# Performance work log

Measured on AMD Instinct MI355X. Metric: run time of the kernel, lower is better.

Reference implementation:

```python
import jax, jax.numpy as jnp
import numpy as np

B, C, H, W, N = 4, 5, 256, 256, 2048
HW = H * W


def setup_inputs() -> dict:
    key = jax.random.key(0)
    ks = jax.random.split(key, 8)
    s = 1.0 / np.sqrt(C)
    x = jax.random.normal(ks[0], (B, C, H, W), jnp.float32)
    Wq = jax.random.normal(ks[1], (C, C), jnp.float32) * s
    Wk = jax.random.normal(ks[2], (C, C), jnp.float32) * s
    Wv = jax.random.normal(ks[3], (C, C), jnp.float32) * s
    bq = jnp.zeros((C,), jnp.float32)
    bk = jnp.zeros((C,), jnp.float32)
    bv = jnp.zeros((C,), jnp.float32)
    gamma = jnp.zeros((1,), jnp.float32)  # nn.Parameter(torch.zeros(1))
    idx_b = jax.random.randint(ks[4], (N,), 0, B, jnp.int32)
    idx_h = jax.random.randint(ks[5], (N,), 0, H, jnp.int32)
    idx_w = jax.random.randint(ks[6], (N,), 0, W, jnp.int32)
    return {"x": x, "Wq": Wq, "bq": bq, "Wk": Wk, "bk": bk, "Wv": Wv,
            "bv": bv, "gamma": gamma, "idx_b": idx_b, "idx_h": idx_h, "idx_w": idx_w}


def _conv1x1(x, Wt, b):
    # 1x1 conv == per-pixel channel mix
    return jnp.einsum('oc,bchw->bohw', Wt, x) + b[None, :, None, None]


def reference(x, Wq, bq, Wk, bk, Wv, bv, gamma, idx_b, idx_h, idx_w):
    q = _conv1x1(x, Wq, bq)
    k = _conv1x1(x, Wk, bk)
    v = _conv1x1(x, Wv, bv)
    q_pix = q[idx_b, :, idx_h, idx_w]              # [N, C] gathered query pixels
    Kf = k.reshape(B, C, HW)
    Vf = v.reshape(B, C, HW)
    # energy[n, l] = sum_c q_pix[n, c] * Kf[idx_b[n], c, l]
    # channel loop (C=5, fixed) avoids materializing [N, C, HW]
    energy = jnp.zeros((N, HW), x.dtype)
    for c in range(C):
        energy = energy + q_pix[:, c:c + 1] * Kf[idx_b, c]   # [N, HW]
    attn = jax.nn.softmax(energy, axis=-1)                   # [N, HW]
    out = jnp.stack([jnp.sum(Vf[idx_b, c] * attn, axis=-1) for c in range(C)],
                    axis=1)                                  # [N, C]
    upd = (gamma[0] + 0.1) * out + x[idx_b, :, idx_h, idx_w]
    # y starts as a detached copy of x; selected pixels are overwritten
    y = jax.lax.stop_gradient(x).at[idx_b, :, idx_h, idx_w].set(upd)
    return y
```

## Files before the change

kernel.cpp:

```cpp
#include <hip/hip_runtime.h>


constexpr int HWC = 256 * 256;
constexpr int Bc  = 4;
constexpr int Nq  = 2048;
constexpr int Wc  = 256;

constexpr int TPB   = 40;
constexpr int SPLIT = 16;

constexpr float LOG2E = 1.4426950408889634f;
constexpr float BIAS2 = -14.0f * LOG2E;

constexpr size_t K8_BYTES  = (size_t)Bc * HWC * 8 * 2;
constexpr size_t VT_BYTES  = (size_t)Bc * 5 * HWC * 2;
constexpr size_t QP_BYTES  = (size_t)Nq * 8 * 2;
constexpr size_t PART_BYTES = (size_t)SPLIT * Nq * 6 * 4;
constexpr size_t K8_OFF   = 0;
constexpr size_t VT_OFF   = K8_OFF + K8_BYTES;
constexpr size_t QP16_OFF = VT_OFF + VT_BYTES;
constexpr size_t PART_OFF = QP16_OFF + QP_BYTES;
constexpr size_t PERM_OFF = PART_OFF + PART_BYTES;
constexpr size_t CNT_OFF  = PERM_OFF + (size_t)Bc * Nq * 4;

typedef __attribute__((ext_vector_type(8))) _Float16 f16x8;
typedef __attribute__((ext_vector_type(4))) float f32x4;
union FU { uint4 u; f16x8 h; };

#if defined(__has_builtin)
#if __has_builtin(__builtin_amdgcn_exp2f)
#define EXP2F(x) __builtin_amdgcn_exp2f(x)
#endif
#endif
#ifndef EXP2F
#define EXP2F(x) exp2f(x)
#endif

__device__ inline unsigned pack2(float a, float b) {
  typedef __attribute__((ext_vector_type(2))) __fp16 fp16x2;
  union { fp16x2 h; unsigned u; } r;
  r.h = __builtin_amdgcn_cvt_pkrtz(a, b);
  return r.u;
}

__global__ __launch_bounds__(256) void k1_prep(
    const float* __restrict__ x,
    const float* __restrict__ Wq, const float* __restrict__ bq,
    const float* __restrict__ Wk, const float* __restrict__ bk,
    const float* __restrict__ Wv, const float* __restrict__ bv,
    const int* __restrict__ idx_b, const int* __restrict__ idx_h,
    const int* __restrict__ idx_w,
    float* __restrict__ y, char* __restrict__ wsb) {
  const int tid = threadIdx.x;
  _Float16* K8   = (_Float16*)(wsb + K8_OFF);
  _Float16* VT   = (_Float16*)(wsb + VT_OFF);
  _Float16* QP16 = (_Float16*)(wsb + QP16_OFF);
  if (blockIdx.x >= 1024) {
    if (blockIdx.x == 1032) {
      __shared__ int lcnt[Bc];
      if (tid < Bc) lcnt[tid] = 0;
      __syncthreads();
      int* perm = (int*)(wsb + PERM_OFF);
#pragma unroll
      for (int qi = 0; qi < 8; ++qi) {
        const int n = qi * 256 + tid;
        const int b = idx_b[n];
        const int pos = atomicAdd(&lcnt[b], 1);
        perm[b * Nq + pos] = n;
      }
      __syncthreads();
      if (tid < Bc) ((int*)(wsb + CNT_OFF))[tid] = lcnt[tid];
      return;
    }
    const int n = (blockIdx.x - 1024) * 256 + tid;
    const int b = idx_b[n];
    const int s = idx_h[n] * Wc + idx_w[n];
    float xv[5];
#pragma unroll
    for (int c = 0; c < 5; ++c) xv[c] = x[(size_t)(b * 5 + c) * HWC + s];
    float q[5];
#pragma unroll
    for (int o = 0; o < 5; ++o) {
      float t = bq[o];
#pragma unroll
      for (int c = 0; c < 5; ++c) t = fmaf(Wq[o * 5 + c], xv[c], t);
      q[o] = t * LOG2E;
    }
    uint4 row;
    row.x = pack2(q[0], q[1]);
    row.y = pack2(q[2], q[3]);
    row.z = pack2(q[4], 0.f);
    row.w = 0u;
    *(uint4*)(QP16 + (size_t)n * 8) = row;
    return;
  }
  const int gid = blockIdx.x * 256 + tid;
  const int b   = gid >> 16;
  const int s   = gid & (HWC - 1);
  float xv[5];
#pragma unroll
  for (int c = 0; c < 5; ++c) {
    const size_t off = (size_t)(b * 5 + c) * HWC + s;
    xv[c] = x[off];
    y[off] = xv[c];
  }
  float kk[5], vv[5];
#pragma unroll
  for (int o = 0; o < 5; ++o) {
    kk[o] = bk[o];
    vv[o] = bv[o];
#pragma unroll
    for (int c = 0; c < 5; ++c) {
      kk[o] = fmaf(Wk[o * 5 + c], xv[c], kk[o]);
      vv[o] = fmaf(Wv[o * 5 + c], xv[c], vv[o]);
    }
  }
  uint4 krow;
  krow.x = pack2(kk[0], kk[1]);
  krow.y = pack2(kk[2], kk[3]);
  krow.z = pack2(kk[4], 0.f);
  krow.w = 0u;
  *(uint4*)(K8 + (size_t)(b * HWC + s) * 8) = krow;
#pragma unroll
  for (int c = 0; c < 5; ++c)
    VT[(size_t)(b * 5 + c) * HWC + s] = (_Float16)vv[c];
}

__global__ __launch_bounds__(256) void k2_attn(char* __restrict__ wsb) {
  const int chunk = blockIdx.x;
  const int tile  = blockIdx.y;
  const int bb    = tile / TPB;
  const int tt    = tile % TPB;
  const int cb    = ((const int*)(wsb + CNT_OFF))[bb];
  const int j0    = tt * 16;
  if (j0 >= cb) return;
  const int* perm = (const int*)(wsb + PERM_OFF) + bb * Nq;

  const int tid  = threadIdx.x;
  const int wv   = tid >> 6;
  const int lane = tid & 63;
  const int quad = lane >> 4;
  const int l15  = lane & 15;

  __shared__ _Float16 Pbuf[4][16][64];
  __shared__ float    Ored[4][16][6];

  const _Float16* K8b  = (const _Float16*)(wsb + K8_OFF) + (size_t)bb * HWC * 8;
  const _Float16* Vtb  = (const _Float16*)(wsb + VT_OFF) + (size_t)bb * 5 * HWC;
  const _Float16* QP16 = (const _Float16*)(wsb + QP16_OFF);

  _Float16* Pw = &Pbuf[wv][0][0];
  const int swzg = 2 * (l15 & 7);
  const int rowb = l15 << 6;
  const int woff0 = rowb + (((0 * 4 + quad) ^ swzg) << 2);
  const int woff1 = rowb + (((1 * 4 + quad) ^ swzg) << 2);
  const int woff2 = rowb + (((2 * 4 + quad) ^ swzg) << 2);
  const int woff3 = rowb + (((3 * 4 + quad) ^ swzg) << 2);
  const int roff0 = rowb + (((0 + 2 * quad) ^ swzg) << 2);
  const int roff1 = rowb + (((8 + 2 * quad) ^ swzg) << 2);

  FU qf; qf.u = make_uint4(0u, 0u, 0u, 0u);
  {
    const int jq = j0 + l15;
    if (quad == 0) {
      const int n = (jq < cb) ? perm[jq] : 0;
      qf.u = *(const uint4*)(QP16 + (size_t)n * 8);
    }
  }
  FU vf0, vf1;
  {
    const unsigned ones = (l15 == 5) ? 0x3C003C00u : 0u;
    vf0.u = make_uint4(ones, ones, ones, ones);
    vf1.u = vf0.u;
  }
  FU kf0, kf1, kf2, kf3;
  kf0.u = make_uint4(0u, 0u, 0u, 0u);
  kf1.u = kf0.u; kf2.u = kf0.u; kf3.u = kf0.u;

  const f32x4 bias = {BIAS2, BIAS2, BIAS2, BIAS2};
  f32x4 oacc = {0.f, 0.f, 0.f, 0.f};

  const _Float16* vplane = Vtb + (size_t)l15 * HWC;

  int s0 = chunk * (HWC / SPLIT) + wv * (HWC / SPLIT / 4);
  for (int it = 0; it < HWC / SPLIT / 4 / 64; ++it, s0 += 64) {
    if (quad == 0) {
      kf0.u = *(const uint4*)(K8b + (size_t)(s0 +  0 + l15) * 8);
      kf1.u = *(const uint4*)(K8b + (size_t)(s0 + 16 + l15) * 8);
      kf2.u = *(const uint4*)(K8b + (size_t)(s0 + 32 + l15) * 8);
      kf3.u = *(const uint4*)(K8b + (size_t)(s0 + 48 + l15) * 8);
    }
    if (l15 < 5) {
      vf0.u = *(const uint4*)(vplane + s0 +  0 + 8 * quad);
      vf1.u = *(const uint4*)(vplane + s0 + 32 + 8 * quad);
    }
    f32x4 e0 = __builtin_amdgcn_mfma_f32_16x16x32_f16(kf0.h, qf.h, bias, 0, 0, 0);
    f32x4 e1 = __builtin_amdgcn_mfma_f32_16x16x32_f16(kf1.h, qf.h, bias, 0, 0, 0);
    f32x4 e2 = __builtin_amdgcn_mfma_f32_16x16x32_f16(kf2.h, qf.h, bias, 0, 0, 0);
    f32x4 e3 = __builtin_amdgcn_mfma_f32_16x16x32_f16(kf3.h, qf.h, bias, 0, 0, 0);
    uint2 w0, w1, w2, w3;
    w0.x = pack2(EXP2F(e0.x), EXP2F(e0.y)); w0.y = pack2(EXP2F(e0.z), EXP2F(e0.w));
    w1.x = pack2(EXP2F(e1.x), EXP2F(e1.y)); w1.y = pack2(EXP2F(e1.z), EXP2F(e1.w));
    w2.x = pack2(EXP2F(e2.x), EXP2F(e2.y)); w2.y = pack2(EXP2F(e2.z), EXP2F(e2.w));
    w3.x = pack2(EXP2F(e3.x), EXP2F(e3.y)); w3.y = pack2(EXP2F(e3.z), EXP2F(e3.w));
    *(uint2*)(Pw + woff0) = w0;
    *(uint2*)(Pw + woff1) = w1;
    *(uint2*)(Pw + woff2) = w2;
    *(uint2*)(Pw + woff3) = w3;
    FU pa0, pa1;
    pa0.h = *(const f16x8*)(Pw + roff0);
    pa1.h = *(const f16x8*)(Pw + roff1);
    oacc = __builtin_amdgcn_mfma_f32_16x16x32_f16(pa0.h, vf0.h, oacc, 0, 0, 0);
    oacc = __builtin_amdgcn_mfma_f32_16x16x32_f16(pa1.h, vf1.h, oacc, 0, 0, 0);
  }

  if (l15 < 6) {
    Ored[wv][4 * quad + 0][l15] = oacc.x;
    Ored[wv][4 * quad + 1][l15] = oacc.y;
    Ored[wv][4 * quad + 2][l15] = oacc.z;
    Ored[wv][4 * quad + 3][l15] = oacc.w;
  }
  __syncthreads();
  if (tid < 96) {
    const int q = tid / 6, comp = tid % 6;
    const float s = Ored[0][q][comp] + Ored[1][q][comp] +
                    Ored[2][q][comp] + Ored[3][q][comp];
    const int j = j0 + q;
    if (j < cb) {
      const int n = perm[j];
      ((float*)(wsb + PART_OFF))[((size_t)chunk * Nq + n) * 6 + comp] = s;
    }
  }
}

__global__ __launch_bounds__(256) void k3_final(
    const float* __restrict__ x, const float* __restrict__ gamma,
    const int* __restrict__ idx_b, const int* __restrict__ idx_h,
    const int* __restrict__ idx_w, float* __restrict__ y,
    const char* __restrict__ wsb) {
  const int n = blockIdx.x * 256 + threadIdx.x;
  const float* part = (const float*)(wsb + PART_OFF);
  float l = 0.f, o[5] = {0.f, 0.f, 0.f, 0.f, 0.f};
#pragma unroll
  for (int ch = 0; ch < SPLIT; ++ch) {
    const float* p = part + ((size_t)ch * Nq + n) * 6;
#pragma unroll
    for (int c = 0; c < 5; ++c) o[c] += p[c];
    l += p[5];
  }
  const float gsc = gamma[0] + 0.1f;
  const float inv = 1.0f / l;
  const int b = idx_b[n], h = idx_h[n], w = idx_w[n];
  const int s = h * Wc + w;
#pragma unroll
  for (int c = 0; c < 5; ++c) {
    const size_t off = (size_t)(b * 5 + c) * HWC + s;
    y[off] = fmaf(gsc, o[c] * inv, x[off]);
  }
}

extern "C" void kernel_launch(void* const* d_in, const int* in_sizes, int n_in,
                              void* d_out, int out_size, void* d_ws, size_t ws_size,
                              hipStream_t stream) {
  const float* x     = (const float*)d_in[0];
  const float* Wq    = (const float*)d_in[1];
  const float* bq    = (const float*)d_in[2];
  const float* Wk    = (const float*)d_in[3];
  const float* bk    = (const float*)d_in[4];
  const float* Wv    = (const float*)d_in[5];
  const float* bv    = (const float*)d_in[6];
  const float* gamma = (const float*)d_in[7];
  const int* idx_b   = (const int*)d_in[8];
  const int* idx_h   = (const int*)d_in[9];
  const int* idx_w   = (const int*)d_in[10];
  float* y  = (float*)d_out;
  char* wsb = (char*)d_ws;

  k1_prep<<<1033, 256, 0, stream>>>(x, Wq, bq, Wk, bk, Wv, bv,
                                    idx_b, idx_h, idx_w, y, wsb);
  k2_attn<<<dim3(SPLIT, Bc * TPB), 256, 0, stream>>>(wsb);
  k3_final<<<Nq / 256, 256, 0, stream>>>(x, gamma, idx_b, idx_h, idx_w, y, wsb);
}
```

Baseline: 118.1 us.

## Software-pipeline K/V register loads in attention loop and raise occupancy hint

The attention inner loop is split into two half-steps, each covering 32 pixels, with A/B register sets. The K and V fragments for the next half-step are loaded while the current half runs its MFMA, exp2 and LDS work, so global load latency overlaps compute. The kernel also gains a launch_bounds minimum of 8 blocks per CU to push the compiler toward fewer registers and higher occupancy. The extra buffered fragments add register pressure, which may conflict with the occupancy hint and cause spills. The last iteration prefetches past each wave's range; these reads are unused but stay inside the workspace.

```diff
diff --git a/kernel.cpp b/kernel.cpp
--- a/kernel.cpp
+++ b/kernel.cpp
@@ -126,7 +126,7 @@
     VT[(size_t)(b * 5 + c) * HWC + s] = (_Float16)vv[c];
 }
 
-__global__ __launch_bounds__(256) void k2_attn(char* __restrict__ wsb) {
+__global__ __launch_bounds__(256, 8) void k2_attn(char* __restrict__ wsb) {
   const int chunk = blockIdx.x;
   const int tile  = blockIdx.y;
   const int bb    = tile / TPB;
@@ -152,12 +152,12 @@
   _Float16* Pw = &Pbuf[wv][0][0];
   const int swzg = 2 * (l15 & 7);
   const int rowb = l15 << 6;
-  const int woff0 = rowb + (((0 * 4 + quad) ^ swzg) << 2);
-  const int woff1 = rowb + (((1 * 4 + quad) ^ swzg) << 2);
-  const int woff2 = rowb + (((2 * 4 + quad) ^ swzg) << 2);
-  const int woff3 = rowb + (((3 * 4 + quad) ^ swzg) << 2);
-  const int roff0 = rowb + (((0 + 2 * quad) ^ swzg) << 2);
-  const int roff1 = rowb + (((8 + 2 * quad) ^ swzg) << 2);
+  const int w0a = rowb + (((0 + quad) ^ swzg) << 2);
+  const int w0b = rowb + (((4 + quad) ^ swzg) << 2);
+  const int r0  = rowb + (((0 + 2 * quad) ^ swzg) << 2);
+  const int w1a = rowb + (((8 + quad) ^ swzg) << 2);
+  const int w1b = rowb + (((12 + quad) ^ swzg) << 2);
+  const int r1  = rowb + (((8 + 2 * quad) ^ swzg) << 2);
 
   FU qf; qf.u = make_uint4(0u, 0u, 0u, 0u);
   {
@@ -167,51 +167,60 @@
       qf.u = *(const uint4*)(QP16 + (size_t)n * 8);
     }
   }
-  FU vf0, vf1;
-  {
-    const unsigned ones = (l15 == 5) ? 0x3C003C00u : 0u;
-    vf0.u = make_uint4(ones, ones, ones, ones);
-    vf1.u = vf0.u;
-  }
-  FU kf0, kf1, kf2, kf3;
-  kf0.u = make_uint4(0u, 0u, 0u, 0u);
-  kf1.u = kf0.u; kf2.u = kf0.u; kf3.u = kf0.u;
+  const unsigned ones = (l15 == 5) ? 0x3C003C00u : 0u;
+
+  FU kA0, kA1, vA, kB0, kB1, vB;
+  kA0.u = make_uint4(0u, 0u, 0u, 0u); kA1.u = kA0.u;
+  kB0.u = kA0.u; kB1.u = kA0.u;
+  vA.u = make_uint4(ones, ones, ones, ones);
+  vB.u = vA.u;
 
   const f32x4 bias = {BIAS2, BIAS2, BIAS2, BIAS2};
   f32x4 oacc = {0.f, 0.f, 0.f, 0.f};
 
   const _Float16* vplane = Vtb + (size_t)l15 * HWC;
 
-  int s0 = chunk * (HWC / SPLIT) + wv * (HWC / SPLIT / 4);
-  for (int it = 0; it < HWC / SPLIT / 4 / 64; ++it, s0 += 64) {
+  int s = chunk * (HWC / SPLIT) + wv * (HWC / SPLIT / 4);
+  if (quad == 0) {
+    kA0.u = *(const uint4*)(K8b + (size_t)(s +  0 + l15) * 8);
+    kA1.u = *(const uint4*)(K8b + (size_t)(s + 16 + l15) * 8);
+  }
+  if (l15 < 5) vA.u = *(const uint4*)(vplane + s + 8 * quad);
+
+  for (int hh = 0; hh < 16; ++hh) {
     if (quad == 0) {
-      kf0.u = *(const uint4*)(K8b + (size_t)(s0 +  0 + l15) * 8);
-      kf1.u = *(const uint4*)(K8b + (size_t)(s0 + 16 + l15) * 8);
-      kf2.u = *(const uint4*)(K8b + (size_t)(s0 + 32 + l15) * 8);
-      kf3.u = *(const uint4*)(K8b + (size_t)(s0 + 48 + l15) * 8);
-    }
-    if (l15 < 5) {
-      vf0.u = *(const uint4*)(vplane + s0 +  0 + 8 * quad);
-      vf1.u = *(const uint4*)(vplane + s0 + 32 + 8 * quad);
-    }
-    f32x4 e0 = __builtin_amdgcn_mfma_f32_16x16x32_f16(kf0.h, qf.h, bias, 0, 0, 0);
-    f32x4 e1 = __builtin_amdgcn_mfma_f32_16x16x32_f16(kf1.h, qf.h, bias, 0, 0, 0);
-    f32x4 e2 = __builtin_amdgcn_mfma_f32_16x16x32_f16(kf2.h, qf.h, bias, 0, 0, 0);
-    f32x4 e3 = __builtin_amdgcn_mfma_f32_16x16x32_f16(kf3.h, qf.h, bias, 0, 0, 0);
-    uint2 w0, w1, w2, w3;
-    w0.x = pack2(EXP2F(e0.x), EXP2F(e0.y)); w0.y = pack2(EXP2F(e0.z), EXP2F(e0.w));
-    w1.x = pack2(EXP2F(e1.x), EXP2F(e1.y)); w1.y = pack2(EXP2F(e1.z), EXP2F(e1.w));
-    w2.x = pack2(EXP2F(e2.x), EXP2F(e2.y)); w2.y = pack2(EXP2F(e2.z), EXP2F(e2.w));
-    w3.x = pack2(EXP2F(e3.x), EXP2F(e3.y)); w3.y = pack2(EXP2F(e3.z), EXP2F(e3.w));
-    *(uint2*)(Pw + woff0) = w0;
-    *(uint2*)(Pw + woff1) = w1;
-    *(uint2*)(Pw + woff2) = w2;
-    *(uint2*)(Pw + woff3) = w3;
-    FU pa0, pa1;
-    pa0.h = *(const f16x8*)(Pw + roff0);
-    pa1.h = *(const f16x8*)(Pw + roff1);
-    oacc = __builtin_amdgcn_mfma_f32_16x16x32_f16(pa0.h, vf0.h, oacc, 0, 0, 0);
-    oacc = __builtin_amdgcn_mfma_f32_16x16x32_f16(pa1.h, vf1.h, oacc, 0, 0, 0);
+      kB0.u = *(const uint4*)(K8b + (size_t)(s + 32 + l15) * 8);
+      kB1.u = *(const uint4*)(K8b + (size_t)(s + 48 + l15) * 8);
+    }
+    if (l15 < 5) vB.u = *(const uint4*)(vplane + s + 32 + 8 * quad);
+    {
+      f32x4 e0 = __builtin_amdgcn_mfma_f32_16x16x32_f16(kA0.h, qf.h, bias, 0, 0, 0);
+      f32x4 e1 = __builtin_amdgcn_mfma_f32_16x16x32_f16(kA1.h, qf.h, bias, 0, 0, 0);
+      uint2 p0, p1;
+      p0.x = pack2(EXP2F(e0.x), EXP2F(e0.y)); p0.y = pack2(EXP2F(e0.z), EXP2F(e0.w));
+      p1.x = pack2(EXP2F(e1.x), EXP2F(e1.y)); p1.y = pack2(EXP2F(e1.z), EXP2F(e1.w));
+      *(uint2*)(Pw + w0a) = p0;
+      *(uint2*)(Pw + w0b) = p1;
+      FU pa; pa.h = *(const f16x8*)(Pw + r0);
+      oacc = __builtin_amdgcn_mfma_f32_16x16x32_f16(pa.h, vA.h, oacc, 0, 0, 0);
+    }
+    if (quad == 0) {
+      kA0.u = *(const uint4*)(K8b + (size_t)(s + 64 + l15) * 8);
+      kA1.u = *(const uint4*)(K8b + (size_t)(s + 80 + l15) * 8);
+    }
+    if (l15 < 5) vA.u = *(const uint4*)(vplane + s + 64 + 8 * quad);
+    {
+      f32x4 e0 = __builtin_amdgcn_mfma_f32_16x16x32_f16(kB0.h, qf.h, bias, 0, 0, 0);
+      f32x4 e1 = __builtin_amdgcn_mfma_f32_16x16x32_f16(kB1.h, qf.h, bias, 0, 0, 0);
+      uint2 p0, p1;
+      p0.x = pack2(EXP2F(e0.x), EXP2F(e0.y)); p0.y = pack2(EXP2F(e0.z), EXP2F(e0.w));
+      p1.x = pack2(EXP2F(e1.x), EXP2F(e1.y)); p1.y = pack2(EXP2F(e1.z), EXP2F(e1.w));
+      *(uint2*)(Pw + w1a) = p0;
+      *(uint2*)(Pw + w1b) = p1;
+      FU pb; pb.h = *(const f16x8*)(Pw + r1);
+      oacc = __builtin_amdgcn_mfma_f32_16x16x32_f16(pb.h, vB.h, oacc, 0, 0, 0);
+    }
+    s += 64;
   }
 
   if (l15 < 6) {
@@ -223,12 +232,12 @@
   __syncthreads();
   if (tid < 96) {
     const int q = tid / 6, comp = tid % 6;
-    const float s = Ored[0][q][comp] + Ored[1][q][comp] +
-                    Ored[2][q][comp] + Ored[3][q][comp];
+    const float sum = Ored[0][q][comp] + Ored[1][q][comp] +
+                      Ored[2][q][comp] + Ored[3][q][comp];
     const int j = j0 + q;
     if (j < cb) {
       const int n = perm[j];
-      ((float*)(wsb + PART_OFF))[((size_t)chunk * Nq + n) * 6 + comp] = s;
+      ((float*)(wsb + PART_OFF))[((size_t)chunk * Nq + n) * 6 + comp] = sum;
     }
   }
 }
```

New measurement: 120.3 us. About the same (+1.9%).
